# Kernel tuning notes

Hardware: AMD Instinct MI355X
Metric: run time of the kernel (lower is better)

The kernel has to match this reference:

```python
import jax, jax.numpy as jnp
import numpy as np

D = 32          # d_model / gcn channels
H_HEADS = 4
HEAD_D = D // H_HEADS
FF = 2048       # TransformerEncoderLayer default dim_feedforward
NUM_CLASSES = 10
EPS = 1e-5


def setup_inputs() -> dict:
    key = jax.random.key(0)
    ks = jax.random.split(key, 24)
    B, Cin, Hh, Ww = 1024, 16, 4, 8          # H*W == 32 (required by reshape into GCN)
    N = B * D                                 # 32768 graph nodes
    E = 2097152                               # ~avg degree 64
    p = lambda k, shp: (jax.random.normal(k, shp, dtype=jnp.float32) * 0.05)
    return {
        "x": jax.random.normal(ks[0], (B, Cin, Hh, Ww), dtype=jnp.float32),
        "edge_index": jax.random.randint(ks[1], (2, E), 0, N, dtype=jnp.int32),
        "conv_w": p(ks[2], (32, Cin, 3, 3)), "conv_b": p(ks[3], (32,)),
        "in_proj_w": p(ks[4], (3 * D, D)), "in_proj_b": p(ks[5], (3 * D,)),
        "out_proj_w": p(ks[6], (D, D)), "out_proj_b": p(ks[7], (D,)),
        "ln1_w": jnp.ones((D,), jnp.float32), "ln1_b": jnp.zeros((D,), jnp.float32),
        "ln2_w": jnp.ones((D,), jnp.float32), "ln2_b": jnp.zeros((D,), jnp.float32),
        "ff1_w": p(ks[8], (FF, D)), "ff1_b": p(ks[9], (FF,)),
        "ff2_w": p(ks[10], (D, FF)), "ff2_b": p(ks[11], (D,)),
        "gcn_w": p(ks[12], (D, D)), "gcn_b": p(ks[13], (D,)),
        "fc_w": p(ks[14], (NUM_CLASSES, D)), "fc_b": p(ks[15], (NUM_CLASSES,)),
    }


def _layernorm(v, w, b):
    m = v.mean(-1, keepdims=True)
    var = v.var(-1, keepdims=True)
    return (v - m) * jax.lax.rsqrt(var + EPS) * w + b


def _gcn(x, row, col, n, w, b):
    # PyG GCNConv: add self-loops, symmetric D^-1/2 (A+I) D^-1/2, x@W^T, + bias
    deg = jax.ops.segment_sum(jnp.ones(row.shape[0], x.dtype), col, num_segments=n)
    dis = jax.lax.rsqrt(jnp.maximum(deg, 1.0))  # self-loops guarantee deg>=1
    norm = dis[row] * dis[col]
    xw = x @ w.T
    msg = xw[row] * norm[:, None]
    return jax.ops.segment_sum(msg, col, num_segments=n) + b


def reference(x, edge_index, conv_w, conv_b, in_proj_w, in_proj_b, out_proj_w,
              out_proj_b, ln1_w, ln1_b, ln2_w, ln2_b, ff1_w, ff1_b, ff2_w, ff2_b,
              gcn_w, gcn_b, fc_w, fc_b):
    # conv2d, padding=1 stride=1 -> SAME
    h = jax.lax.conv_general_dilated(x, conv_w, (1, 1), "SAME",
                                     dimension_numbers=("NCHW", "OIHW", "NCHW"))
    h = h + conv_b[None, :, None, None]
    B, C, Hh, Ww = h.shape
    z = h.reshape(B, C, Hh * Ww).transpose(0, 2, 1)  # (B, HW, 32)

    # torch TransformerEncoderLayer, batch_first=False: axis0=seq(B), axis1=batch(HW)
    qkv = z @ in_proj_w.T + in_proj_b                 # (S, Nb, 3D)
    q, k, v = jnp.split(qkv, 3, axis=-1)
    S, Nb = z.shape[0], z.shape[1]
    rs = lambda t: t.reshape(S, Nb, H_HEADS, HEAD_D)
    q, k, v = rs(q), rs(k), rs(v)
    scores = jnp.einsum("snhd,tnhd->nhst", q, k) / np.sqrt(HEAD_D).astype(np.float32)
    attn = jax.nn.softmax(scores, axis=-1)
    o = jnp.einsum("nhst,tnhd->snhd", attn, v).reshape(S, Nb, D)
    o = o @ out_proj_w.T + out_proj_b
    z = _layernorm(z + o, ln1_w, ln1_b)               # post-norm (torch default)
    ff = jax.nn.relu(z @ ff1_w.T + ff1_b) @ ff2_w.T + ff2_b
    z = _layernorm(z + ff, ln2_w, ln2_b)

    # (B, HW, 32) -> (B, 32, HW) -> (B*32, HW) ; HW == 32 so GCN in_channels match
    g = z.transpose(0, 2, 1).reshape(B * C, Hh * Ww)
    n = g.shape[0]
    loops = jnp.arange(n, dtype=edge_index.dtype)
    row = jnp.concatenate([edge_index[0], loops])
    col = jnp.concatenate([edge_index[1], loops])
    g = _gcn(g, row, col, n, gcn_w, gcn_b)
    g = jax.nn.relu(g)  # dropout is identity in eval mode
    g = _gcn(g, row, col, n, gcn_w, gcn_b)            # shared weights (same module)
    logits = g @ fc_w.T + fc_b
    return jax.nn.log_softmax(logits, axis=1)
```

## Files before the change

### kernel.cpp

```cpp
#include <hip/hip_runtime.h>

#define NTOK 32768

__global__ __launch_bounds__(256) void conv_kernel(
    const float* __restrict__ x, const float* __restrict__ w,
    const float* __restrict__ bias, float* __restrict__ z) {
  __shared__ float xs[16 * 32];
  __shared__ float wsm[32 * 145];
  __shared__ float bs[32];
  int b = blockIdx.x, tid = threadIdx.x;
  const float* xb = x + b * 512;
  for (int i = tid; i < 512; i += 256) xs[i] = xb[i];
  for (int i = tid; i < 4608; i += 256) wsm[(i / 144) * 145 + (i % 144)] = w[i];
  if (tid < 32) bs[tid] = bias[tid];
  __syncthreads();
  #pragma unroll
  for (int r = 0; r < 4; ++r) {
    int oid = r * 256 + tid;
    int co = oid & 31, pos = oid >> 5;
    int y = pos >> 3, xx = pos & 7;
    float acc = bs[co];
    const float* wr = &wsm[co * 145];
    for (int ci = 0; ci < 16; ++ci) {
      #pragma unroll
      for (int ky = 0; ky < 3; ++ky) {
        int yy = y + ky - 1;
        if (yy < 0 || yy > 3) continue;
        #pragma unroll
        for (int kx = 0; kx < 3; ++kx) {
          int xc = xx + kx - 1;
          if (xc < 0 || xc > 7) continue;
          acc += xs[ci * 32 + yy * 8 + xc] * wr[ci * 9 + ky * 3 + kx];
        }
      }
    }
    z[(b * 32 + pos) * 32 + co] = acc;
  }
}

__global__ __launch_bounds__(256) void qkv_kernel(
    const float* __restrict__ z, const float* __restrict__ W,
    const float* __restrict__ bias, float* __restrict__ qt,
    float* __restrict__ kt, float* __restrict__ vt) {
  __shared__ float wsm[96 * 32];
  __shared__ float bs[96];
  int tid = threadIdx.x;
  for (int i = tid; i < 3072; i += 256) wsm[i] = W[i];
  if (tid < 96) bs[tid] = bias[tid];
  __syncthreads();
  int s = tid >> 3, bl = tid & 7;
  int b = blockIdx.x * 8 + bl;
  int token = b * 32 + s;
  float zr[32];
  const float4* zp = (const float4*)(z + token * 32);
  #pragma unroll
  for (int i = 0; i < 8; ++i) {
    float4 v = zp[i];
    zr[i * 4 + 0] = v.x; zr[i * 4 + 1] = v.y; zr[i * 4 + 2] = v.z; zr[i * 4 + 3] = v.w;
  }
  for (int part = 0; part < 3; ++part) {
    float* dst = part == 0 ? qt : (part == 1 ? kt : vt);
    for (int hh = 0; hh < 4; ++hh) {
      float out[8];
      #pragma unroll
      for (int j = 0; j < 8; ++j) {
        int jj = part * 32 + hh * 8 + j;
        float a = bs[jj];
        const float* wr = &wsm[jj * 32];
        #pragma unroll
        for (int k = 0; k < 32; ++k) a += zr[k] * wr[k];
        out[j] = a;
      }
      float4* p = (float4*)(dst + ((size_t)(s * 4 + hh) * 1024 + b) * 8);
      p[0] = make_float4(out[0], out[1], out[2], out[3]);
      p[1] = make_float4(out[4], out[5], out[6], out[7]);
    }
  }
}

__global__ __launch_bounds__(256) void attn_kernel(
    const float* __restrict__ qt, const float* __restrict__ kt,
    const float* __restrict__ vt, float* __restrict__ o) {
  __shared__ __align__(16) float Ks[1024 * 8];
  __shared__ __align__(16) float Vs[1024 * 8];
  int slab = blockIdx.x >> 2, qc = blockIdx.x & 3;
  int tid = threadIdx.x;
  const float4* kp = (const float4*)(kt + (size_t)slab * 8192);
  const float4* vp = (const float4*)(vt + (size_t)slab * 8192);
  float4* ksp = (float4*)Ks;
  float4* vsp = (float4*)Vs;
  for (int i = tid; i < 2048; i += 256) { ksp[i] = kp[i]; vsp[i] = vp[i]; }
  __syncthreads();
  int b = qc * 256 + tid;
  const float4* qp = (const float4*)(qt + ((size_t)slab * 1024 + b) * 8);
  float4 q0 = qp[0], q1 = qp[1];
  const float scale = 0.35355339059327373f;
  q0.x *= scale; q0.y *= scale; q0.z *= scale; q0.w *= scale;
  q1.x *= scale; q1.y *= scale; q1.z *= scale; q1.w *= scale;
  float m = -1e30f;
  for (int t = 0; t < 1024; ++t) {
    const float4* kk = (const float4*)&Ks[t * 8];
    float4 k0 = kk[0], k1 = kk[1];
    float s = q0.x * k0.x + q0.y * k0.y + q0.z * k0.z + q0.w * k0.w +
              q1.x * k1.x + q1.y * k1.y + q1.z * k1.z + q1.w * k1.w;
    m = fmaxf(m, s);
  }
  float l = 0.f;
  float a0 = 0, a1 = 0, a2 = 0, a3 = 0, a4 = 0, a5 = 0, a6 = 0, a7 = 0;
  for (int t = 0; t < 1024; ++t) {
    const float4* kk = (const float4*)&Ks[t * 8];
    float4 k0 = kk[0], k1 = kk[1];
    float s = q0.x * k0.x + q0.y * k0.y + q0.z * k0.z + q0.w * k0.w +
              q1.x * k1.x + q1.y * k1.y + q1.z * k1.z + q1.w * k1.w;
    float p = __expf(s - m);
    l += p;
    const float4* vv = (const float4*)&Vs[t * 8];
    float4 v0 = vv[0], v1 = vv[1];
    a0 += p * v0.x; a1 += p * v0.y; a2 += p * v0.z; a3 += p * v0.w;
    a4 += p * v1.x; a5 += p * v1.y; a6 += p * v1.z; a7 += p * v1.w;
  }
  float inv = 1.f / l;
  int npos = slab >> 2, hh = slab & 3;
  float4* op = (float4*)(o + ((size_t)(b * 32 + npos)) * 32 + hh * 8);
  op[0] = make_float4(a0 * inv, a1 * inv, a2 * inv, a3 * inv);
  op[1] = make_float4(a4 * inv, a5 * inv, a6 * inv, a7 * inv);
}

__global__ __launch_bounds__(256) void proj_ln1_kernel(
    const float* __restrict__ z, const float* __restrict__ o,
    const float* __restrict__ W, const float* __restrict__ bias,
    const float* __restrict__ lw, const float* __restrict__ lb,
    float* __restrict__ zn1) {
  __shared__ float wsm[1024];
  __shared__ float bs[32], lws[32], lbs[32];
  int tid = threadIdx.x;
  for (int i = tid; i < 1024; i += 256) wsm[i] = W[i];
  if (tid < 32) { bs[tid] = bias[tid]; lws[tid] = lw[tid]; lbs[tid] = lb[tid]; }
  __syncthreads();
  int token = blockIdx.x * 256 + tid;
  float orow[32], zrow[32], v[32];
  const float4* opnt = (const float4*)(o + (size_t)token * 32);
  const float4* zp = (const float4*)(z + (size_t)token * 32);
  #pragma unroll
  for (int i = 0; i < 8; ++i) {
    float4 t4 = opnt[i];
    orow[i * 4] = t4.x; orow[i * 4 + 1] = t4.y; orow[i * 4 + 2] = t4.z; orow[i * 4 + 3] = t4.w;
    float4 z4 = zp[i];
    zrow[i * 4] = z4.x; zrow[i * 4 + 1] = z4.y; zrow[i * 4 + 2] = z4.z; zrow[i * 4 + 3] = z4.w;
  }
  float s1 = 0.f, s2 = 0.f;
  for (int j = 0; j < 32; ++j) {
    float a = bs[j];
    const float* wr = &wsm[j * 32];
    #pragma unroll
    for (int k = 0; k < 32; ++k) a += orow[k] * wr[k];
    float t = a + zrow[j];
    v[j] = t; s1 += t; s2 += t * t;
  }
  float mean = s1 * (1.f / 32.f);
  float var = s2 * (1.f / 32.f) - mean * mean;
  float rs = rsqrtf(var + 1e-5f);
  float4* dst = (float4*)(zn1 + (size_t)token * 32);
  #pragma unroll
  for (int k4 = 0; k4 < 8; ++k4) {
    float4 ov;
    ov.x = (v[k4 * 4 + 0] - mean) * rs * lws[k4 * 4 + 0] + lbs[k4 * 4 + 0];
    ov.y = (v[k4 * 4 + 1] - mean) * rs * lws[k4 * 4 + 1] + lbs[k4 * 4 + 1];
    ov.z = (v[k4 * 4 + 2] - mean) * rs * lws[k4 * 4 + 2] + lbs[k4 * 4 + 2];
    ov.w = (v[k4 * 4 + 3] - mean) * rs * lws[k4 * 4 + 3] + lbs[k4 * 4 + 3];
    dst[k4] = ov;
  }
}

__global__ __launch_bounds__(256, 2) void ffn_kernel(
    const float* __restrict__ zn1, const float* __restrict__ w1,
    const float* __restrict__ b1, const float* __restrict__ w2,
    const float* __restrict__ b2, const float* __restrict__ lw,
    const float* __restrict__ lb, float* __restrict__ zn2) {
  __shared__ __align__(16) float w1s[128 * 36];
  __shared__ __align__(16) float w2s[128 * 36];
  __shared__ float b1s[128];
  __shared__ float lws[32], lbs[32], b2s[32];
  int tid = threadIdx.x;
  int p = tid >> 3, fg = tid & 7;
  int t0 = blockIdx.x * 64 + p * 2;
  float z0[32], z1[32], acc0[32], acc1[32];
  const float4* zp0 = (const float4*)(zn1 + (size_t)t0 * 32);
  const float4* zp1 = (const float4*)(zn1 + (size_t)(t0 + 1) * 32);
  #pragma unroll
  for (int i = 0; i < 8; ++i) {
    float4 a = zp0[i];
    z0[i * 4 + 0] = a.x; z0[i * 4 + 1] = a.y; z0[i * 4 + 2] = a.z; z0[i * 4 + 3] = a.w;
    float4 b = zp1[i];
    z1[i * 4 + 0] = b.x; z1[i * 4 + 1] = b.y; z1[i * 4 + 2] = b.z; z1[i * 4 + 3] = b.w;
  }
  #pragma unroll
  for (int d = 0; d < 32; ++d) { acc0[d] = 0.f; acc1[d] = 0.f; }
  if (tid < 32) { lws[tid] = lw[tid]; lbs[tid] = lb[tid]; b2s[tid] = b2[tid]; }
  for (int ch = 0; ch < 16; ++ch) {
    __syncthreads();
    #pragma unroll
    for (int pass = 0; pass < 4; ++pass) {
      int idx = pass * 256 + tid;
      int fr = idx >> 3, k4 = idx & 7;
      float4 v = ((const float4*)(w1 + (size_t)(ch * 128 + fr) * 32))[k4];
      float* dptr = &w1s[fr * 36 + k4 * 4];
      dptr[0] = v.x; dptr[1] = v.y; dptr[2] = v.z; dptr[3] = v.w;
    }
    #pragma unroll
    for (int pass = 0; pass < 4; ++pass) {
      int idx = pass * 256 + tid;
      int dd = idx >> 5, f4 = idx & 31;
      float4 v = ((const float4*)(w2 + (size_t)dd * 2048 + ch * 128))[f4];
      w2s[(f4 * 4 + 0) * 36 + dd] = v.x;
      w2s[(f4 * 4 + 1) * 36 + dd] = v.y;
      w2s[(f4 * 4 + 2) * 36 + dd] = v.z;
      w2s[(f4 * 4 + 3) * 36 + dd] = v.w;
    }
    if (tid < 128) b1s[tid] = b1[ch * 128 + tid];
    __syncthreads();
    #pragma unroll 4
    for (int i = 0; i < 16; ++i) {
      int f = i * 8 + fg;
      const float4* wr = (const float4*)&w1s[f * 36];
      float h0 = b1s[f], h1 = h0;
      #pragma unroll
      for (int k4 = 0; k4 < 8; ++k4) {
        float4 wv = wr[k4];
        h0 += z0[k4 * 4 + 0] * wv.x + z0[k4 * 4 + 1] * wv.y + z0[k4 * 4 + 2] * wv.z + z0[k4 * 4 + 3] * wv.w;
        h1 += z1[k4 * 4 + 0] * wv.x + z1[k4 * 4 + 1] * wv.y + z1[k4 * 4 + 2] * wv.z + z1[k4 * 4 + 3] * wv.w;
      }
      h0 = fmaxf(h0, 0.f); h1 = fmaxf(h1, 0.f);
      const float4* vr = (const float4*)&w2s[f * 36];
      #pragma unroll
      for (int d4 = 0; d4 < 8; ++d4) {
        float4 vv = vr[d4];
        acc0[d4 * 4 + 0] += h0 * vv.x; acc0[d4 * 4 + 1] += h0 * vv.y;
        acc0[d4 * 4 + 2] += h0 * vv.z; acc0[d4 * 4 + 3] += h0 * vv.w;
        acc1[d4 * 4 + 0] += h1 * vv.x; acc1[d4 * 4 + 1] += h1 * vv.y;
        acc1[d4 * 4 + 2] += h1 * vv.z; acc1[d4 * 4 + 3] += h1 * vv.w;
      }
    }
  }
  #pragma unroll
  for (int d = 0; d < 32; ++d) {
    float a = acc0[d];
    a += __shfl_xor(a, 1); a += __shfl_xor(a, 2); a += __shfl_xor(a, 4);
    acc0[d] = a;
    float b = acc1[d];
    b += __shfl_xor(b, 1); b += __shfl_xor(b, 2); b += __shfl_xor(b, 4);
    acc1[d] = b;
  }
  if (fg == 0) {
    float v[32];
    float s1 = 0.f, s2 = 0.f;
    #pragma unroll
    for (int d = 0; d < 32; ++d) {
      float t = z0[d] + acc0[d] + b2s[d];
      v[d] = t; s1 += t; s2 += t * t;
    }
    float mean = s1 * (1.f / 32.f);
    float var = s2 * (1.f / 32.f) - mean * mean;
    float rs = rsqrtf(var + 1e-5f);
    float4* dst = (float4*)(zn2 + (size_t)t0 * 32);
    #pragma unroll
    for (int k4 = 0; k4 < 8; ++k4) {
      float4 ov;
      ov.x = (v[k4 * 4 + 0] - mean) * rs * lws[k4 * 4 + 0] + lbs[k4 * 4 + 0];
      ov.y = (v[k4 * 4 + 1] - mean) * rs * lws[k4 * 4 + 1] + lbs[k4 * 4 + 1];
      ov.z = (v[k4 * 4 + 2] - mean) * rs * lws[k4 * 4 + 2] + lbs[k4 * 4 + 2];
      ov.w = (v[k4 * 4 + 3] - mean) * rs * lws[k4 * 4 + 3] + lbs[k4 * 4 + 3];
      dst[k4] = ov;
    }
    float s1b = 0.f, s2b = 0.f;
    #pragma unroll
    for (int d = 0; d < 32; ++d) {
      float t = z1[d] + acc1[d] + b2s[d];
      v[d] = t; s1b += t; s2b += t * t;
    }
    mean = s1b * (1.f / 32.f);
    var = s2b * (1.f / 32.f) - mean * mean;
    rs = rsqrtf(var + 1e-5f);
    dst = (float4*)(zn2 + (size_t)(t0 + 1) * 32);
    #pragma unroll
    for (int k4 = 0; k4 < 8; ++k4) {
      float4 ov;
      ov.x = (v[k4 * 4 + 0] - mean) * rs * lws[k4 * 4 + 0] + lbs[k4 * 4 + 0];
      ov.y = (v[k4 * 4 + 1] - mean) * rs * lws[k4 * 4 + 1] + lbs[k4 * 4 + 1];
      ov.z = (v[k4 * 4 + 2] - mean) * rs * lws[k4 * 4 + 2] + lbs[k4 * 4 + 2];
      ov.w = (v[k4 * 4 + 3] - mean) * rs * lws[k4 * 4 + 3] + lbs[k4 * 4 + 3];
      dst[k4] = ov;
    }
  }
}

__global__ __launch_bounds__(256) void transpose_kernel(
    const float* __restrict__ zn2, float* __restrict__ g) {
  __shared__ float t[32 * 33];
  int b = blockIdx.x, tid = threadIdx.x;
  const float* src = zn2 + (size_t)b * 1024;
  #pragma unroll
  for (int l = 0; l < 4; ++l) {
    int o_ = l * 256 + tid;
    t[(o_ >> 5) * 33 + (o_ & 31)] = src[o_];
  }
  __syncthreads();
  float* dst = g + (size_t)b * 1024;
  #pragma unroll
  for (int l = 0; l < 4; ++l) {
    int o_ = l * 256 + tid;
    int c = o_ >> 5, s = o_ & 31;
    dst[o_] = t[s * 33 + c];
  }
}

__global__ void degi_kernel(const int* __restrict__ col, int* __restrict__ degi, int E) {
  int e = blockIdx.x * 256 + threadIdx.x;
  if (e < E) atomicAdd(&degi[col[e]], 1);
}

__global__ __launch_bounds__(1024) void scan_kernel(
    const int* __restrict__ degi, int* __restrict__ offs, int* __restrict__ cur,
    float* __restrict__ dis, int E) {
  __shared__ int ts[1024];
  int tid = threadIdx.x;
  int base = tid * 32;
  int loc[32];
  int s = 0;
  #pragma unroll
  for (int i = 0; i < 32; ++i) { loc[i] = s; s += degi[base + i]; }
  ts[tid] = s;
  __syncthreads();
  for (int d = 1; d < 1024; d <<= 1) {
    int v = (tid >= d) ? ts[tid - d] : 0;
    __syncthreads();
    ts[tid] += v;
    __syncthreads();
  }
  int excl = (tid == 0) ? 0 : ts[tid - 1];
  #pragma unroll
  for (int i = 0; i < 32; ++i) {
    int o = excl + loc[i];
    offs[base + i] = o;
    cur[base + i] = o;
    dis[base + i] = rsqrtf((float)(degi[base + i] + 1));
  }
  if (tid == 1023) offs[NTOK] = E;
}

__global__ void fill_kernel(const int* __restrict__ row, const int* __restrict__ col,
                            const float* __restrict__ dis, int* __restrict__ cur,
                            int2* __restrict__ erec, int E) {
  int e = blockIdx.x * 256 + threadIdx.x;
  if (e >= E) return;
  int r = row[e], c = col[e];
  int slot = atomicAdd(&cur[c], 1);
  float nrm = dis[r] * dis[c];
  erec[slot] = make_int2(r, __float_as_int(nrm));
}

__global__ __launch_bounds__(256) void gcn_in_kernel(
    const float* __restrict__ g, const float* __restrict__ w,
    float* __restrict__ xw) {
  __shared__ float wsm[1024];
  int tid = threadIdx.x;
  for (int i = tid; i < 1024; i += 256) wsm[i] = w[i];
  __syncthreads();
  int n = blockIdx.x * 256 + tid;
  float gr[32];
  const float4* gp = (const float4*)(g + (size_t)n * 32);
  #pragma unroll
  for (int i = 0; i < 8; ++i) {
    float4 v = gp[i];
    gr[i * 4] = v.x; gr[i * 4 + 1] = v.y; gr[i * 4 + 2] = v.z; gr[i * 4 + 3] = v.w;
  }
  float4* xp = (float4*)(xw + (size_t)n * 32);
  for (int d4 = 0; d4 < 8; ++d4) {
    float o_[4];
    #pragma unroll
    for (int j = 0; j < 4; ++j) {
      const float* wr = &wsm[(d4 * 4 + j) * 32];
      float a = 0.f;
      #pragma unroll
      for (int k = 0; k < 32; ++k) a += gr[k] * wr[k];
      o_[j] = a;
    }
    xp[d4] = make_float4(o_[0], o_[1], o_[2], o_[3]);
  }
}

__global__ __launch_bounds__(256) void gather_kernel(
    const float* __restrict__ xw, const float* __restrict__ dis,
    const int* __restrict__ offs, const int2* __restrict__ erec,
    float* __restrict__ agg) {
  int gid = blockIdx.x * 256 + threadIdx.x;
  int c = gid >> 3, q = gid & 7;
  int start = offs[c], end = offs[c + 1];
  float dn = dis[c];
  float dn2 = dn * dn;
  float4 self = ((const float4*)(xw + (size_t)c * 32))[q];
  float a0 = self.x * dn2, a1 = self.y * dn2, a2 = self.z * dn2, a3 = self.w * dn2;
  int e = start;
  #pragma unroll 4
  for (; e < end; ++e) {
    int2 rec = erec[e];
    float nrm = __int_as_float(rec.y);
    float4 v = ((const float4*)(xw + (size_t)rec.x * 32))[q];
    a0 += v.x * nrm; a1 += v.y * nrm; a2 += v.z * nrm; a3 += v.w * nrm;
  }
  ((float4*)(agg + (size_t)c * 32))[q] = make_float4(a0, a1, a2, a3);
}

__global__ __launch_bounds__(256) void gcn_mid_kernel(
    const float* __restrict__ agg, const float* __restrict__ gb,
    const float* __restrict__ w, float* __restrict__ xw2) {
  __shared__ float wsm[1024];
  __shared__ float bs[32];
  int tid = threadIdx.x;
  for (int i = tid; i < 1024; i += 256) wsm[i] = w[i];
  if (tid < 32) bs[tid] = gb[tid];
  __syncthreads();
  int n = blockIdx.x * 256 + tid;
  float gr[32];
  const float4* ap = (const float4*)(agg + (size_t)n * 32);
  #pragma unroll
  for (int i = 0; i < 8; ++i) {
    float4 v = ap[i];
    gr[i * 4 + 0] = fmaxf(v.x + bs[i * 4 + 0], 0.f);
    gr[i * 4 + 1] = fmaxf(v.y + bs[i * 4 + 1], 0.f);
    gr[i * 4 + 2] = fmaxf(v.z + bs[i * 4 + 2], 0.f);
    gr[i * 4 + 3] = fmaxf(v.w + bs[i * 4 + 3], 0.f);
  }
  float4* xp = (float4*)(xw2 + (size_t)n * 32);
  for (int d4 = 0; d4 < 8; ++d4) {
    float o_[4];
    #pragma unroll
    for (int j = 0; j < 4; ++j) {
      const float* wr = &wsm[(d4 * 4 + j) * 32];
      float a = 0.f;
      #pragma unroll
      for (int k = 0; k < 32; ++k) a += gr[k] * wr[k];
      o_[j] = a;
    }
    xp[d4] = make_float4(o_[0], o_[1], o_[2], o_[3]);
  }
}

__global__ __launch_bounds__(256) void gcn_out_kernel(
    const float* __restrict__ agg2, const float* __restrict__ gb,
    const float* __restrict__ fw, const float* __restrict__ fb,
    float* __restrict__ out) {
  __shared__ float wsm[320];
  __shared__ float bs[10];
  __shared__ float gbs[32];
  int tid = threadIdx.x;
  for (int i = tid; i < 320; i += 256) wsm[i] = fw[i];
  if (tid < 10) bs[tid] = fb[tid];
  if (tid < 32) gbs[tid] = gb[tid];
  __syncthreads();
  int n = blockIdx.x * 256 + tid;
  float v[32];
  const float4* ap = (const float4*)(agg2 + (size_t)n * 32);
  #pragma unroll
  for (int i = 0; i < 8; ++i) {
    float4 t4 = ap[i];
    v[i * 4 + 0] = t4.x + gbs[i * 4 + 0];
    v[i * 4 + 1] = t4.y + gbs[i * 4 + 1];
    v[i * 4 + 2] = t4.z + gbs[i * 4 + 2];
    v[i * 4 + 3] = t4.w + gbs[i * 4 + 3];
  }
  float lg[10];
  float mx = -1e30f;
  for (int j = 0; j < 10; ++j) {
    float a = bs[j];
    const float* wr = &wsm[j * 32];
    #pragma unroll
    for (int k = 0; k < 32; ++k) a += v[k] * wr[k];
    lg[j] = a;
    mx = fmaxf(mx, a);
  }
  float se = 0.f;
  for (int j = 0; j < 10; ++j) se += __expf(lg[j] - mx);
  float ls = logf(se);
  for (int j = 0; j < 10; ++j) out[(size_t)n * 10 + j] = lg[j] - mx - ls;
}

extern "C" void kernel_launch(void* const* d_in, const int* in_sizes, int n_in,
                              void* d_out, int out_size, void* d_ws, size_t ws_size,
                              hipStream_t stream) {
  const float* x      = (const float*)d_in[0];
  const int*   ei     = (const int*)d_in[1];
  const float* conv_w = (const float*)d_in[2];
  const float* conv_b = (const float*)d_in[3];
  const float* in_w   = (const float*)d_in[4];
  const float* in_b   = (const float*)d_in[5];
  const float* out_w  = (const float*)d_in[6];
  const float* out_b  = (const float*)d_in[7];
  const float* ln1_w  = (const float*)d_in[8];
  const float* ln1_b  = (const float*)d_in[9];
  const float* ln2_w  = (const float*)d_in[10];
  const float* ln2_b  = (const float*)d_in[11];
  const float* ff1_w  = (const float*)d_in[12];
  const float* ff1_b  = (const float*)d_in[13];
  const float* ff2_w  = (const float*)d_in[14];
  const float* ff2_b  = (const float*)d_in[15];
  const float* gcn_w  = (const float*)d_in[16];
  const float* gcn_b  = (const float*)d_in[17];
  const float* fc_w   = (const float*)d_in[18];
  const float* fc_b   = (const float*)d_in[19];
  int E = in_sizes[1] / 2;
  const int* rowp = ei;
  const int* colp = ei + E;

  float* wsf = (float*)d_ws;
  const size_t M = 1048576;
  float* Z   = wsf + 0 * M;
  float* QT  = wsf + 1 * M;
  float* KT  = wsf + 2 * M;
  float* VT  = wsf + 3 * M;
  float* O   = wsf + 4 * M;
  float* ZN1 = wsf + 5 * M;
  float* ZN2 = wsf + 6 * M;
  int*   DEGI = (int*)(wsf + 7 * M);
  int*   OFFS = DEGI + 32768;
  int*   CUR  = OFFS + 32770;
  float* DIS  = (float*)(CUR + 32768);
  int2*  EREC = (int2*)(DIS + 32768);
  float* G   = QT;
  float* XW  = KT;
  float* AGG = VT;
  float* XW2 = O;
  float* AG2 = Z;

  conv_kernel<<<1024, 256, 0, stream>>>(x, conv_w, conv_b, Z);
  qkv_kernel<<<128, 256, 0, stream>>>(Z, in_w, in_b, QT, KT, VT);
  attn_kernel<<<512, 256, 0, stream>>>(QT, KT, VT, O);
  proj_ln1_kernel<<<128, 256, 0, stream>>>(Z, O, out_w, out_b, ln1_w, ln1_b, ZN1);
  ffn_kernel<<<512, 256, 0, stream>>>(ZN1, ff1_w, ff1_b, ff2_w, ff2_b, ln2_w, ln2_b, ZN2);
  transpose_kernel<<<1024, 256, 0, stream>>>(ZN2, G);
  hipMemsetAsync(DEGI, 0, 32768 * sizeof(int), stream);
  degi_kernel<<<(E + 255) / 256, 256, 0, stream>>>(colp, DEGI, E);
  scan_kernel<<<1, 1024, 0, stream>>>(DEGI, OFFS, CUR, DIS, E);
  fill_kernel<<<(E + 255) / 256, 256, 0, stream>>>(rowp, colp, DIS, CUR, EREC, E);
  gcn_in_kernel<<<128, 256, 0, stream>>>(G, gcn_w, XW);
  gather_kernel<<<1024, 256, 0, stream>>>(XW, DIS, OFFS, EREC, AGG);
  gcn_mid_kernel<<<128, 256, 0, stream>>>(AGG, gcn_b, gcn_w, XW2);
  gather_kernel<<<1024, 256, 0, stream>>>(XW2, DIS, OFFS, EREC, AG2);
  gcn_out_kernel<<<128, 256, 0, stream>>>(AG2, gcn_b, fc_w, fc_b, (float*)d_out);
}
```

Baseline: 800.3 us.

## Fuse GCN stages, drop softmax max pass, retile FFN, fold memset into conv

Merges the transpose with the first GCN linear, and each gather with the following linear or the classifier plus log-softmax, using warp shuffles to reduce across the 8 lanes per node. This removes several launches and intermediate round trips through global memory. The attention softmax loses its max-subtraction pass, which halves the key loop but risks overflow in exp when scores are large. The FFN now uses 16 lanes per token pair with higher occupancy bounds, and the degree-buffer zeroing moves into the conv kernel instead of a memset.

```diff
diff --git a/kernel.cpp b/kernel.cpp
--- a/kernel.cpp
+++ b/kernel.cpp
@@ -4,11 +4,13 @@
 
 __global__ __launch_bounds__(256) void conv_kernel(
     const float* __restrict__ x, const float* __restrict__ w,
-    const float* __restrict__ bias, float* __restrict__ z) {
+    const float* __restrict__ bias, float* __restrict__ z,
+    int* __restrict__ degi) {
   __shared__ float xs[16 * 32];
   __shared__ float wsm[32 * 145];
   __shared__ float bs[32];
   int b = blockIdx.x, tid = threadIdx.x;
+  if (b < 128) degi[b * 256 + tid] = 0;
   const float* xb = x + b * 512;
   for (int i = tid; i < 512; i += 256) xs[i] = xb[i];
   for (int i = tid; i < 4608; i += 256) wsm[(i / 144) * 145 + (i % 144)] = w[i];
@@ -97,22 +99,15 @@
   const float scale = 0.35355339059327373f;
   q0.x *= scale; q0.y *= scale; q0.z *= scale; q0.w *= scale;
   q1.x *= scale; q1.y *= scale; q1.z *= scale; q1.w *= scale;
-  float m = -1e30f;
+  float l = 0.f;
+  float a0 = 0, a1 = 0, a2 = 0, a3 = 0, a4 = 0, a5 = 0, a6 = 0, a7 = 0;
+  #pragma unroll 4
   for (int t = 0; t < 1024; ++t) {
     const float4* kk = (const float4*)&Ks[t * 8];
     float4 k0 = kk[0], k1 = kk[1];
     float s = q0.x * k0.x + q0.y * k0.y + q0.z * k0.z + q0.w * k0.w +
               q1.x * k1.x + q1.y * k1.y + q1.z * k1.z + q1.w * k1.w;
-    m = fmaxf(m, s);
-  }
-  float l = 0.f;
-  float a0 = 0, a1 = 0, a2 = 0, a3 = 0, a4 = 0, a5 = 0, a6 = 0, a7 = 0;
-  for (int t = 0; t < 1024; ++t) {
-    const float4* kk = (const float4*)&Ks[t * 8];
-    float4 k0 = kk[0], k1 = kk[1];
-    float s = q0.x * k0.x + q0.y * k0.y + q0.z * k0.z + q0.w * k0.w +
-              q1.x * k1.x + q1.y * k1.y + q1.z * k1.z + q1.w * k1.w;
-    float p = __expf(s - m);
+    float p = __expf(s);
     l += p;
     const float4* vv = (const float4*)&Vs[t * 8];
     float4 v0 = vv[0], v1 = vv[1];
@@ -172,7 +167,7 @@
   }
 }
 
-__global__ __launch_bounds__(256, 2) void ffn_kernel(
+__global__ __launch_bounds__(256, 4) void ffn_kernel(
     const float* __restrict__ zn1, const float* __restrict__ w1,
     const float* __restrict__ b1, const float* __restrict__ w2,
     const float* __restrict__ b2, const float* __restrict__ lw,
@@ -182,8 +177,8 @@
   __shared__ float b1s[128];
   __shared__ float lws[32], lbs[32], b2s[32];
   int tid = threadIdx.x;
-  int p = tid >> 3, fg = tid & 7;
-  int t0 = blockIdx.x * 64 + p * 2;
+  int p = tid >> 4, fg = tid & 15;
+  int t0 = blockIdx.x * 32 + p * 2;
   float z0[32], z1[32], acc0[32], acc1[32];
   const float4* zp0 = (const float4*)(zn1 + (size_t)t0 * 32);
   const float4* zp1 = (const float4*)(zn1 + (size_t)(t0 + 1) * 32);
@@ -220,8 +215,8 @@
     if (tid < 128) b1s[tid] = b1[ch * 128 + tid];
     __syncthreads();
     #pragma unroll 4
-    for (int i = 0; i < 16; ++i) {
-      int f = i * 8 + fg;
+    for (int i = 0; i < 8; ++i) {
+      int f = i * 16 + fg;
       const float4* wr = (const float4*)&w1s[f * 36];
       float h0 = b1s[f], h1 = h0;
       #pragma unroll
@@ -245,10 +240,10 @@
   #pragma unroll
   for (int d = 0; d < 32; ++d) {
     float a = acc0[d];
-    a += __shfl_xor(a, 1); a += __shfl_xor(a, 2); a += __shfl_xor(a, 4);
+    a += __shfl_xor(a, 1); a += __shfl_xor(a, 2); a += __shfl_xor(a, 4); a += __shfl_xor(a, 8);
     acc0[d] = a;
     float b = acc1[d];
-    b += __shfl_xor(b, 1); b += __shfl_xor(b, 2); b += __shfl_xor(b, 4);
+    b += __shfl_xor(b, 1); b += __shfl_xor(b, 2); b += __shfl_xor(b, 4); b += __shfl_xor(b, 8);
     acc1[d] = b;
   }
   if (fg == 0) {
@@ -294,23 +289,38 @@
   }
 }
 
-__global__ __launch_bounds__(256) void transpose_kernel(
-    const float* __restrict__ zn2, float* __restrict__ g) {
-  __shared__ float t[32 * 33];
-  int b = blockIdx.x, tid = threadIdx.x;
-  const float* src = zn2 + (size_t)b * 1024;
-  #pragma unroll
-  for (int l = 0; l < 4; ++l) {
-    int o_ = l * 256 + tid;
-    t[(o_ >> 5) * 33 + (o_ & 31)] = src[o_];
-  }
-  __syncthreads();
-  float* dst = g + (size_t)b * 1024;
-  #pragma unroll
-  for (int l = 0; l < 4; ++l) {
-    int o_ = l * 256 + tid;
-    int c = o_ >> 5, s = o_ & 31;
-    dst[o_] = t[s * 33 + c];
+__global__ __launch_bounds__(256) void tgcn_kernel(
+    const float* __restrict__ zn2, const float* __restrict__ w,
+    float* __restrict__ xw) {
+  __shared__ float ts[8 * 1056];
+  __shared__ float wsm[1024];
+  int tid = threadIdx.x;
+  for (int i = tid; i < 1024; i += 256) wsm[i] = w[i];
+  const float* src = zn2 + (size_t)blockIdx.x * 8192;
+  #pragma unroll
+  for (int l = 0; l < 32; ++l) {
+    int o = l * 256 + tid;
+    int bl = o >> 10, s = (o >> 5) & 31, c = o & 31;
+    ts[bl * 1056 + s * 33 + c] = src[o];
+  }
+  __syncthreads();
+  int bl = tid >> 5, c = tid & 31;
+  float gr[32];
+  #pragma unroll
+  for (int k = 0; k < 32; ++k) gr[k] = ts[bl * 1056 + k * 33 + c];
+  int n = blockIdx.x * 256 + tid;
+  float4* xp = (float4*)(xw + (size_t)n * 32);
+  for (int d4 = 0; d4 < 8; ++d4) {
+    float o_[4];
+    #pragma unroll
+    for (int j = 0; j < 4; ++j) {
+      const float* wr = &wsm[(d4 * 4 + j) * 32];
+      float a = 0.f;
+      #pragma unroll
+      for (int k = 0; k < 32; ++k) a += gr[k] * wr[k];
+      o_[j] = a;
+    }
+    xp[d4] = make_float4(o_[0], o_[1], o_[2], o_[3]);
   }
 }
 
@@ -359,130 +369,106 @@
   erec[slot] = make_int2(r, __float_as_int(nrm));
 }
 
-__global__ __launch_bounds__(256) void gcn_in_kernel(
-    const float* __restrict__ g, const float* __restrict__ w,
-    float* __restrict__ xw) {
-  __shared__ float wsm[1024];
-  int tid = threadIdx.x;
-  for (int i = tid; i < 1024; i += 256) wsm[i] = w[i];
-  __syncthreads();
-  int n = blockIdx.x * 256 + tid;
-  float gr[32];
-  const float4* gp = (const float4*)(g + (size_t)n * 32);
-  #pragma unroll
-  for (int i = 0; i < 8; ++i) {
-    float4 v = gp[i];
-    gr[i * 4] = v.x; gr[i * 4 + 1] = v.y; gr[i * 4 + 2] = v.z; gr[i * 4 + 3] = v.w;
-  }
-  float4* xp = (float4*)(xw + (size_t)n * 32);
-  for (int d4 = 0; d4 < 8; ++d4) {
-    float o_[4];
-    #pragma unroll
-    for (int j = 0; j < 4; ++j) {
-      const float* wr = &wsm[(d4 * 4 + j) * 32];
-      float a = 0.f;
-      #pragma unroll
-      for (int k = 0; k < 32; ++k) a += gr[k] * wr[k];
-      o_[j] = a;
-    }
-    xp[d4] = make_float4(o_[0], o_[1], o_[2], o_[3]);
-  }
-}
-
-__global__ __launch_bounds__(256) void gather_kernel(
+__global__ __launch_bounds__(256) void gather_mid_kernel(
     const float* __restrict__ xw, const float* __restrict__ dis,
     const int* __restrict__ offs, const int2* __restrict__ erec,
-    float* __restrict__ agg) {
-  int gid = blockIdx.x * 256 + threadIdx.x;
+    const float* __restrict__ gb, const float* __restrict__ w,
+    float* __restrict__ xw2) {
+  __shared__ float wsm[1024];
+  __shared__ float bs[32];
+  int tid = threadIdx.x;
+  for (int i = tid; i < 1024; i += 256) wsm[i] = w[i];
+  if (tid < 32) bs[tid] = gb[tid];
+  __syncthreads();
+  int gid = blockIdx.x * 256 + tid;
   int c = gid >> 3, q = gid & 7;
   int start = offs[c], end = offs[c + 1];
   float dn = dis[c];
   float dn2 = dn * dn;
   float4 self = ((const float4*)(xw + (size_t)c * 32))[q];
   float a0 = self.x * dn2, a1 = self.y * dn2, a2 = self.z * dn2, a3 = self.w * dn2;
-  int e = start;
   #pragma unroll 4
-  for (; e < end; ++e) {
+  for (int e = start; e < end; ++e) {
     int2 rec = erec[e];
     float nrm = __int_as_float(rec.y);
     float4 v = ((const float4*)(xw + (size_t)rec.x * 32))[q];
     a0 += v.x * nrm; a1 += v.y * nrm; a2 += v.z * nrm; a3 += v.w * nrm;
   }
-  ((float4*)(agg + (size_t)c * 32))[q] = make_float4(a0, a1, a2, a3);
-}
-
-__global__ __launch_bounds__(256) void gcn_mid_kernel(
-    const float* __restrict__ agg, const float* __restrict__ gb,
-    const float* __restrict__ w, float* __restrict__ xw2) {
-  __shared__ float wsm[1024];
-  __shared__ float bs[32];
-  int tid = threadIdx.x;
-  for (int i = tid; i < 1024; i += 256) wsm[i] = w[i];
-  if (tid < 32) bs[tid] = gb[tid];
-  __syncthreads();
-  int n = blockIdx.x * 256 + tid;
-  float gr[32];
-  const float4* ap = (const float4*)(agg + (size_t)n * 32);
-  #pragma unroll
-  for (int i = 0; i < 8; ++i) {
-    float4 v = ap[i];
-    gr[i * 4 + 0] = fmaxf(v.x + bs[i * 4 + 0], 0.f);
-    gr[i * 4 + 1] = fmaxf(v.y + bs[i * 4 + 1], 0.f);
-    gr[i * 4 + 2] = fmaxf(v.z + bs[i * 4 + 2], 0.f);
-    gr[i * 4 + 3] = fmaxf(v.w + bs[i * 4 + 3], 0.f);
-  }
-  float4* xp = (float4*)(xw2 + (size_t)n * 32);
-  for (int d4 = 0; d4 < 8; ++d4) {
-    float o_[4];
-    #pragma unroll
-    for (int j = 0; j < 4; ++j) {
-      const float* wr = &wsm[(d4 * 4 + j) * 32];
-      float a = 0.f;
-      #pragma unroll
-      for (int k = 0; k < 32; ++k) a += gr[k] * wr[k];
-      o_[j] = a;
-    }
-    xp[d4] = make_float4(o_[0], o_[1], o_[2], o_[3]);
-  }
-}
-
-__global__ __launch_bounds__(256) void gcn_out_kernel(
-    const float* __restrict__ agg2, const float* __restrict__ gb,
-    const float* __restrict__ fw, const float* __restrict__ fb,
-    float* __restrict__ out) {
-  __shared__ float wsm[320];
-  __shared__ float bs[10];
+  float r0 = fmaxf(a0 + bs[q * 4 + 0], 0.f);
+  float r1 = fmaxf(a1 + bs[q * 4 + 1], 0.f);
+  float r2 = fmaxf(a2 + bs[q * 4 + 2], 0.f);
+  float r3 = fmaxf(a3 + bs[q * 4 + 3], 0.f);
+  float part[32];
+  #pragma unroll
+  for (int d = 0; d < 32; ++d) {
+    float4 wv = *(const float4*)&wsm[d * 32 + q * 4];
+    part[d] = wv.x * r0 + wv.y * r1 + wv.z * r2 + wv.w * r3;
+  }
+  #pragma unroll
+  for (int d = 0; d < 32; ++d) {
+    float a = part[d];
+    a += __shfl_xor(a, 1); a += __shfl_xor(a, 2); a += __shfl_xor(a, 4);
+    part[d] = a;
+  }
+  ((float4*)(xw2 + (size_t)c * 32))[q] =
+      make_float4(part[q * 4 + 0], part[q * 4 + 1], part[q * 4 + 2], part[q * 4 + 3]);
+}
+
+__global__ __launch_bounds__(256) void gather_out_kernel(
+    const float* __restrict__ xw2, const float* __restrict__ dis,
+    const int* __restrict__ offs, const int2* __restrict__ erec,
+    const float* __restrict__ gb, const float* __restrict__ fw,
+    const float* __restrict__ fb, float* __restrict__ out) {
+  __shared__ float fws[320];
+  __shared__ float fbs[10];
   __shared__ float gbs[32];
   int tid = threadIdx.x;
-  for (int i = tid; i < 320; i += 256) wsm[i] = fw[i];
-  if (tid < 10) bs[tid] = fb[tid];
+  for (int i = tid; i < 320; i += 256) fws[i] = fw[i];
+  if (tid < 10) fbs[tid] = fb[tid];
   if (tid < 32) gbs[tid] = gb[tid];
   __syncthreads();
-  int n = blockIdx.x * 256 + tid;
-  float v[32];
-  const float4* ap = (const float4*)(agg2 + (size_t)n * 32);
-  #pragma unroll
-  for (int i = 0; i < 8; ++i) {
-    float4 t4 = ap[i];
-    v[i * 4 + 0] = t4.x + gbs[i * 4 + 0];
-    v[i * 4 + 1] = t4.y + gbs[i * 4 + 1];
-    v[i * 4 + 2] = t4.z + gbs[i * 4 + 2];
-    v[i * 4 + 3] = t4.w + gbs[i * 4 + 3];
-  }
+  int gid = blockIdx.x * 256 + tid;
+  int c = gid >> 3, q = gid & 7;
+  int start = offs[c], end = offs[c + 1];
+  float dn = dis[c];
+  float dn2 = dn * dn;
+  float4 self = ((const float4*)(xw2 + (size_t)c * 32))[q];
+  float a0 = self.x * dn2, a1 = self.y * dn2, a2 = self.z * dn2, a3 = self.w * dn2;
+  #pragma unroll 4
+  for (int e = start; e < end; ++e) {
+    int2 rec = erec[e];
+    float nrm = __int_as_float(rec.y);
+    float4 v = ((const float4*)(xw2 + (size_t)rec.x * 32))[q];
+    a0 += v.x * nrm; a1 += v.y * nrm; a2 += v.z * nrm; a3 += v.w * nrm;
+  }
+  float v0 = a0 + gbs[q * 4 + 0];
+  float v1 = a1 + gbs[q * 4 + 1];
+  float v2 = a2 + gbs[q * 4 + 2];
+  float v3 = a3 + gbs[q * 4 + 3];
   float lg[10];
-  float mx = -1e30f;
+  #pragma unroll
   for (int j = 0; j < 10; ++j) {
-    float a = bs[j];
-    const float* wr = &wsm[j * 32];
-    #pragma unroll
-    for (int k = 0; k < 32; ++k) a += v[k] * wr[k];
+    float4 wv = *(const float4*)&fws[j * 32 + q * 4];
+    lg[j] = wv.x * v0 + wv.y * v1 + wv.z * v2 + wv.w * v3;
+  }
+  #pragma unroll
+  for (int j = 0; j < 10; ++j) {
+    float a = lg[j];
+    a += __shfl_xor(a, 1); a += __shfl_xor(a, 2); a += __shfl_xor(a, 4);
     lg[j] = a;
-    mx = fmaxf(mx, a);
-  }
-  float se = 0.f;
-  for (int j = 0; j < 10; ++j) se += __expf(lg[j] - mx);
-  float ls = logf(se);
-  for (int j = 0; j < 10; ++j) out[(size_t)n * 10 + j] = lg[j] - mx - ls;
+  }
+  if (q == 0) {
+    float mx = -1e30f;
+    #pragma unroll
+    for (int j = 0; j < 10; ++j) { lg[j] += fbs[j]; mx = fmaxf(mx, lg[j]); }
+    float se = 0.f;
+    #pragma unroll
+    for (int j = 0; j < 10; ++j) se += __expf(lg[j] - mx);
+    float ls = logf(se);
+    float* op = out + (size_t)c * 10;
+    #pragma unroll
+    for (int j = 0; j < 10; ++j) op[j] = lg[j] - mx - ls;
+  }
 }
 
 extern "C" void kernel_launch(void* const* d_in, const int* in_sizes, int n_in,
@@ -526,25 +512,18 @@
   int*   CUR  = OFFS + 32770;
   float* DIS  = (float*)(CUR + 32768);
   int2*  EREC = (int2*)(DIS + 32768);
-  float* G   = QT;
   float* XW  = KT;
-  float* AGG = VT;
   float* XW2 = O;
-  float* AG2 = Z;
-
-  conv_kernel<<<1024, 256, 0, stream>>>(x, conv_w, conv_b, Z);
+
+  conv_kernel<<<1024, 256, 0, stream>>>(x, conv_w, conv_b, Z, DEGI);
   qkv_kernel<<<128, 256, 0, stream>>>(Z, in_w, in_b, QT, KT, VT);
   attn_kernel<<<512, 256, 0, stream>>>(QT, KT, VT, O);
   proj_ln1_kernel<<<128, 256, 0, stream>>>(Z, O, out_w, out_b, ln1_w, ln1_b, ZN1);
-  ffn_kernel<<<512, 256, 0, stream>>>(ZN1, ff1_w, ff1_b, ff2_w, ff2_b, ln2_w, ln2_b, ZN2);
-  transpose_kernel<<<1024, 256, 0, stream>>>(ZN2, G);
-  hipMemsetAsync(DEGI, 0, 32768 * sizeof(int), stream);
+  ffn_kernel<<<1024, 256, 0, stream>>>(ZN1, ff1_w, ff1_b, ff2_w, ff2_b, ln2_w, ln2_b, ZN2);
   degi_kernel<<<(E + 255) / 256, 256, 0, stream>>>(colp, DEGI, E);
   scan_kernel<<<1, 1024, 0, stream>>>(DEGI, OFFS, CUR, DIS, E);
   fill_kernel<<<(E + 255) / 256, 256, 0, stream>>>(rowp, colp, DIS, CUR, EREC, E);
-  gcn_in_kernel<<<128, 256, 0, stream>>>(G, gcn_w, XW);
-  gather_kernel<<<1024, 256, 0, stream>>>(XW, DIS, OFFS, EREC, AGG);
-  gcn_mid_kernel<<<128, 256, 0, stream>>>(AGG, gcn_b, gcn_w, XW2);
-  gather_kernel<<<1024, 256, 0, stream>>>(XW2, DIS, OFFS, EREC, AG2);
-  gcn_out_kernel<<<128, 256, 0, stream>>>(AG2, gcn_b, fc_w, fc_b, (float*)d_out);
-}
+  tgcn_kernel<<<128, 256, 0, stream>>>(ZN2, gcn_w, XW);
+  gather_mid_kernel<<<1024, 256, 0, stream>>>(XW, DIS, OFFS, EREC, gcn_b, gcn_w, XW2);
+  gather_out_kernel<<<1024, 256, 0, stream>>>(XW2, DIS, OFFS, EREC, gcn_b, fc_w, fc_b, (float*)d_out);
+}
```

Result: slower. 1.583 ms (+97.8%).
